# Kernel tuning notes

Measured on AMD Instinct MI355X. Metric: run time of the kernel, lower is better.

## Reference

```python
import jax, jax.numpy as jnp
import numpy as np

D_MODEL = 1024
N_HEADS = 16
HEAD_DIM = D_MODEL // N_HEADS
MASKED_BIAS = -10000.0


def setup_inputs() -> dict:
    key = jax.random.key(0)
    k1, k2, k3 = jax.random.split(key, 3)
    B, S = 2, 2048
    hidden_states = jax.random.normal(k1, (B, S, D_MODEL), dtype=jnp.float32)
    c_attn_w = jax.random.normal(k2, (D_MODEL, 3 * D_MODEL), dtype=jnp.float32) * 0.02
    c_attn_b = jnp.zeros((3 * D_MODEL,), dtype=jnp.float32)
    c_proj_w = jax.random.normal(k3, (D_MODEL, D_MODEL), dtype=jnp.float32) * 0.02
    c_proj_b = jnp.zeros((D_MODEL,), dtype=jnp.float32)
    return {
        "hidden_states": hidden_states,
        "c_attn_w": c_attn_w,
        "c_attn_b": c_attn_b,
        "c_proj_w": c_proj_w,
        "c_proj_b": c_proj_b,
    }


def reference(hidden_states, c_attn_w, c_attn_b, c_proj_w, c_proj_b):
    B, S, D = hidden_states.shape
    qkv = hidden_states @ c_attn_w + c_attn_b  # [B, S, 3D]
    q, k, v = jnp.split(qkv, 3, axis=-1)
    # split heads -> [B, H, S, Dh]
    def split_heads(t):
        return t.reshape(B, S, N_HEADS, HEAD_DIM).transpose(0, 2, 1, 3)
    q, k, v = split_heads(q), split_heads(k), split_heads(v)
    attn_weights = jnp.einsum("bhqd,bhkd->bhqk", q, k)
    attn_weights = attn_weights / jnp.asarray(float(HEAD_DIM) ** 0.5, attn_weights.dtype)
    causal_mask = jnp.tril(jnp.ones((S, S), dtype=bool))[None, None]
    attn_weights = jnp.where(causal_mask, attn_weights, jnp.asarray(MASKED_BIAS, attn_weights.dtype))
    attn_weights = jax.nn.softmax(attn_weights, axis=-1)
    attn_output = jnp.einsum("bhqk,bhkd->bhqd", attn_weights, v)
    attn_output = attn_output.transpose(0, 2, 1, 3).reshape(B, S, D)
    attn_output = attn_output @ c_proj_w + c_proj_b
    return attn_output, attn_weights
```

## Files before the change

### kernel.cpp

```cpp
#include <hip/hip_runtime.h>
#include <hip/hip_bf16.h>

#define BB 2
#define SS 2048
#define DD 1024
#define HH 16
#define DH 64
#define N3 3072

typedef __hip_bfloat16 bf16;
typedef __attribute__((ext_vector_type(8))) short short8;
typedef __attribute__((ext_vector_type(4))) short short4v;
typedef __attribute__((ext_vector_type(4))) float f32x4;

__device__ __forceinline__ float b2f(bf16 x) { return __bfloat162float(x); }

__device__ __forceinline__ short f2bs(float x) {
    bf16 t = __float2bfloat16(x);
    return *reinterpret_cast<short*>(&t);
}

__global__ __launch_bounds__(256) void split_f32(const float* __restrict__ x,
                                                 bf16* __restrict__ hi,
                                                 bf16* __restrict__ lo, int n4) {
    int idx = blockIdx.x * 256 + threadIdx.x;
    const int stride = gridDim.x * 256;
    for (int i = idx; i < n4; i += stride) {
        f32x4 v = ((const f32x4*)x)[i];
        short4v h, l;
        #pragma unroll
        for (int j = 0; j < 4; ++j) {
            bf16 hh = __float2bfloat16(v[j]);
            h[j] = *reinterpret_cast<short*>(&hh);
            float lof = v[j] - b2f(hh);
            l[j] = f2bs(lof);
        }
        ((short4v*)hi)[i] = h;
        ((short4v*)lo)[i] = l;
    }
}

__global__ __launch_bounds__(256) void transpose_split(const float* __restrict__ W,
                                                       bf16* __restrict__ Th,
                                                       bf16* __restrict__ Tl,
                                                       int K, int N) {
    __shared__ float t[64][65];
    const int k0 = blockIdx.y * 64, n0 = blockIdx.x * 64;
    const int c = threadIdx.x & 63, r4 = threadIdx.x >> 6;
    #pragma unroll
    for (int i = 0; i < 16; ++i) {
        int r = i * 4 + r4;
        t[r][c] = W[(size_t)(k0 + r) * N + n0 + c];
    }
    __syncthreads();
    #pragma unroll
    for (int i = 0; i < 16; ++i) {
        int r = i * 4 + r4;
        float x = t[c][r];
        bf16 h = __float2bfloat16(x);
        float lof = x - b2f(h);
        Th[(size_t)(n0 + r) * K + k0 + c] = h;
        Tl[(size_t)(n0 + r) * K + k0 + c] = __float2bfloat16(lof);
    }
}

__global__ __launch_bounds__(256) void qkv_mfma(const bf16* __restrict__ Ah,
                                                const bf16* __restrict__ Al,
                                                const bf16* __restrict__ Bh,
                                                const bf16* __restrict__ Bl,
                                                const float* __restrict__ bias,
                                                bf16* __restrict__ Qh,
                                                bf16* __restrict__ Kh,
                                                bf16* __restrict__ Vt) {
    const int nwg = (N3 / 128) * ((BB * SS) / 128);
    const int orig = blockIdx.x;
    const int swz = (orig & 7) * (nwg >> 3) + (orig >> 3);
    const int bx = swz % (N3 / 128), by = swz / (N3 / 128);
    const int m0 = by * 128, n0 = bx * 128;

    const int tid = threadIdx.x;
    const int lane = tid & 63;
    const int w = tid >> 6;
    const int wr = w >> 1, wc = w & 1;
    const int g = lane >> 4, lr = lane & 15;

    f32x4 acc[4][4];
    #pragma unroll
    for (int i = 0; i < 4; ++i)
        #pragma unroll
        for (int j = 0; j < 4; ++j) acc[i][j] = (f32x4){0.f, 0.f, 0.f, 0.f};

    const size_t arow = (size_t)(m0 + wr * 64 + lr) * DD;
    const size_t brow = (size_t)(n0 + wc * 64 + lr) * DD;

    for (int k0 = 0; k0 < DD; k0 += 32) {
        const int ko = k0 + g * 8;
        short8 ah[4], al[4], bhf[4], blf[4];
        #pragma unroll
        for (int i = 0; i < 4; ++i) {
            ah[i] = *(const short8*)(Ah + arow + (size_t)i * 16 * DD + ko);
            al[i] = *(const short8*)(Al + arow + (size_t)i * 16 * DD + ko);
        }
        #pragma unroll
        for (int j = 0; j < 4; ++j) {
            bhf[j] = *(const short8*)(Bh + brow + (size_t)j * 16 * DD + ko);
            blf[j] = *(const short8*)(Bl + brow + (size_t)j * 16 * DD + ko);
        }
        #pragma unroll
        for (int i = 0; i < 4; ++i)
            #pragma unroll
            for (int j = 0; j < 4; ++j) {
                acc[i][j] = __builtin_amdgcn_mfma_f32_16x16x32_bf16(ah[i], bhf[j], acc[i][j], 0, 0, 0);
                acc[i][j] = __builtin_amdgcn_mfma_f32_16x16x32_bf16(ah[i], blf[j], acc[i][j], 0, 0, 0);
                acc[i][j] = __builtin_amdgcn_mfma_f32_16x16x32_bf16(al[i], bhf[j], acc[i][j], 0, 0, 0);
            }
    }

    #pragma unroll
    for (int j = 0; j < 4; ++j) {
        const int n = n0 + wc * 64 + j * 16 + lr;
        const float bn = bias[n];
        const int which = n >> 10;
        const int d = n & 1023;
        const int h = d >> 6, dh = d & 63;
        #pragma unroll
        for (int i = 0; i < 4; ++i) {
            #pragma unroll
            for (int r = 0; r < 4; ++r) {
                const int m = m0 + wr * 64 + i * 16 + g * 4 + r;
                const int b_ = m >> 11, s = m & 2047;
                const int bh = b_ * HH + h;
                const float v = acc[i][j][r] + bn;
                if (which == 0) {
                    Qh[((size_t)bh * SS + s) * DH + dh] = __float2bfloat16(v * 0.125f);
                } else if (which == 1) {
                    Kh[((size_t)bh * SS + s) * DH + dh] = __float2bfloat16(v);
                } else {
                    Vt[((size_t)bh * DH + dh) * SS + s] = __float2bfloat16(v);
                }
            }
        }
    }
}

__global__ __launch_bounds__(64) void attn_mfma(const bf16* __restrict__ Qh,
                                                const bf16* __restrict__ Kh,
                                                const bf16* __restrict__ Vt,
                                                float* __restrict__ Wout,
                                                bf16* __restrict__ Hh) {
    const int lane = threadIdx.x;
    const int g = lane >> 4;
    const int lr = lane & 15;
    const int idx = blockIdx.x;
    const int bh = idx & 31;
    const int t = 127 - (idx >> 5);
    const int qw = t * 16;
    const int nkt = (t >> 2) + 1;

    __shared__ short pb16[1024];
    char* pb = (char*)pb16;

    short8 qf0, qf1;
    {
        const bf16* qp = Qh + ((size_t)bh * SS + qw + lr) * DH + g * 8;
        qf0 = *(const short8*)(qp);
        qf1 = *(const short8*)(qp + 32);
    }

    float lsum[4] = {0.f, 0.f, 0.f, 0.f};
    for (int kt = 0; kt < nkt; ++kt) {
        const int kbase = kt * 64;
        const bf16* kt_ptr = Kh + ((size_t)bh * SS + kbase) * DH;
        const bool diag = (kt == nkt - 1);
        f32x4 acc[4];
        #pragma unroll
        for (int ct = 0; ct < 4; ++ct) {
            const bf16* kp = kt_ptr + (size_t)(ct * 16 + lr) * DH + g * 8;
            short8 b0 = *(const short8*)(kp);
            short8 b1 = *(const short8*)(kp + 32);
            f32x4 a = {0.f, 0.f, 0.f, 0.f};
            a = __builtin_amdgcn_mfma_f32_16x16x32_bf16(qf0, b0, a, 0, 0, 0);
            a = __builtin_amdgcn_mfma_f32_16x16x32_bf16(qf1, b1, a, 0, 0, 0);
            acc[ct] = a;
        }
        #pragma unroll
        for (int r = 0; r < 4; ++r) {
            const int qrow = qw + g * 4 + r;
            float e = 0.f;
            #pragma unroll
            for (int ct = 0; ct < 4; ++ct) {
                float ev = __expf(acc[ct][r]);
                if (diag && (kbase + ct * 16 + lr) > qrow) ev = 0.f;
                e += ev;
            }
            lsum[r] += e;
        }
    }
    float inv[4];
    #pragma unroll
    for (int r = 0; r < 4; ++r) {
        float s = lsum[r];
        s += __shfl_xor(s, 1, 64);
        s += __shfl_xor(s, 2, 64);
        s += __shfl_xor(s, 4, 64);
        s += __shfl_xor(s, 8, 64);
        inv[r] = 1.f / s;
    }

    f32x4 oacc[4];
    #pragma unroll
    for (int ct = 0; ct < 4; ++ct) oacc[ct] = (f32x4){0.f, 0.f, 0.f, 0.f};

    const size_t wbase = ((size_t)bh * SS + qw) * SS;

    for (int kt = 0; kt < nkt; ++kt) {
        const int kbase = kt * 64;
        const bf16* kt_ptr = Kh + ((size_t)bh * SS + kbase) * DH;
        const bool diag = (kt == nkt - 1);
        #pragma unroll
        for (int ct = 0; ct < 4; ++ct) {
            const bf16* kp = kt_ptr + (size_t)(ct * 16 + lr) * DH + g * 8;
            short8 b0 = *(const short8*)(kp);
            short8 b1 = *(const short8*)(kp + 32);
            f32x4 a = {0.f, 0.f, 0.f, 0.f};
            a = __builtin_amdgcn_mfma_f32_16x16x32_bf16(qf0, b0, a, 0, 0, 0);
            a = __builtin_amdgcn_mfma_f32_16x16x32_bf16(qf1, b1, a, 0, 0, 0);
            #pragma unroll
            for (int r = 0; r < 4; ++r) {
                const int qrow = qw + g * 4 + r;
                const int kcol = kbase + ct * 16 + lr;
                float p = __expf(a[r]) * inv[r];
                if (diag && kcol > qrow) p = 0.f;
                Wout[wbase + (size_t)(g * 4 + r) * SS + kcol] = p;
                const int row = g * 4 + r;
                const int byte = row * 128 +
                                 (((ct * 16 + lr) * 2) ^ ((row & 7) << 4));
                *(short*)(pb + byte) = f2bs(p);
            }
        }
        __syncthreads();
        short8 pf0 = *(short8*)(pb + lr * 128 + ((g * 16) ^ ((lr & 7) << 4)));
        short8 pf1 = *(short8*)(pb + lr * 128 + ((64 + g * 16) ^ ((lr & 7) << 4)));
        const bf16* vbase = Vt + (size_t)bh * DH * SS + kbase;
        #pragma unroll
        for (int ct = 0; ct < 4; ++ct) {
            const bf16* vp = vbase + (size_t)(ct * 16 + lr) * SS + g * 8;
            short8 v0 = *(const short8*)(vp);
            short8 v1 = *(const short8*)(vp + 32);
            oacc[ct] = __builtin_amdgcn_mfma_f32_16x16x32_bf16(pf0, v0, oacc[ct], 0, 0, 0);
            oacc[ct] = __builtin_amdgcn_mfma_f32_16x16x32_bf16(pf1, v1, oacc[ct], 0, 0, 0);
        }
        __syncthreads();
    }

    #pragma unroll
    for (int ct = 0; ct < 4; ++ct) {
        #pragma unroll
        for (int r = 0; r < 4; ++r) {
            const int qrow = qw + g * 4 + r;
            const int dh = ct * 16 + lr;
            Hh[((size_t)bh * SS + qrow) * DH + dh] = __float2bfloat16(oacc[ct][r]);
        }
    }

    const int kend = nkt * 64;
    const f32x4 z = {0.f, 0.f, 0.f, 0.f};
    #pragma unroll
    for (int s = 0; s < 4; ++s) {
        const int row = (lane >> 4) + 4 * s;
        float* wr = Wout + wbase + (size_t)row * SS;
        for (int c = kend + (lane & 15) * 4; c < SS; c += 64)
            *(f32x4*)(wr + c) = z;
    }
}

__global__ __launch_bounds__(256) void proj_mfma(const bf16* __restrict__ Hh,
                                                 const bf16* __restrict__ Bh,
                                                 const bf16* __restrict__ Bl,
                                                 const float* __restrict__ bias,
                                                 float* __restrict__ out) {
    const int nwg = (DD / 128) * ((BB * SS) / 128);
    const int orig = blockIdx.x;
    const int swz = (orig & 7) * (nwg >> 3) + (orig >> 3);
    const int bx = swz % (DD / 128), by = swz / (DD / 128);
    const int m0 = by * 128, n0 = bx * 128;

    const int tid = threadIdx.x;
    const int lane = tid & 63;
    const int w = tid >> 6;
    const int wr = w >> 1, wc = w & 1;
    const int g = lane >> 4, lr = lane & 15;

    f32x4 acc[4][4];
    #pragma unroll
    for (int i = 0; i < 4; ++i)
        #pragma unroll
        for (int j = 0; j < 4; ++j) acc[i][j] = (f32x4){0.f, 0.f, 0.f, 0.f};

    const size_t brow = (size_t)(n0 + wc * 64 + lr) * DD;

    for (int k0 = 0; k0 < DD; k0 += 32) {
        const int ko = k0 + g * 8;
        const int h = ko >> 6, dho = ko & 63;
        short8 af[4], bhf[4], blf[4];
        #pragma unroll
        for (int i = 0; i < 4; ++i) {
            const int m = m0 + wr * 64 + i * 16 + lr;
            const bf16* ap = Hh + (((size_t)(m >> 11) * HH + h) * SS + (m & 2047)) * DH + dho;
            af[i] = *(const short8*)ap;
        }
        #pragma unroll
        for (int j = 0; j < 4; ++j) {
            bhf[j] = *(const short8*)(Bh + brow + (size_t)j * 16 * DD + ko);
            blf[j] = *(const short8*)(Bl + brow + (size_t)j * 16 * DD + ko);
        }
        #pragma unroll
        for (int i = 0; i < 4; ++i)
            #pragma unroll
            for (int j = 0; j < 4; ++j) {
                acc[i][j] = __builtin_amdgcn_mfma_f32_16x16x32_bf16(af[i], bhf[j], acc[i][j], 0, 0, 0);
                acc[i][j] = __builtin_amdgcn_mfma_f32_16x16x32_bf16(af[i], blf[j], acc[i][j], 0, 0, 0);
            }
    }

    #pragma unroll
    for (int j = 0; j < 4; ++j) {
        const int n = n0 + wc * 64 + j * 16 + lr;
        const float bn = bias[n];
        #pragma unroll
        for (int i = 0; i < 4; ++i) {
            #pragma unroll
            for (int r = 0; r < 4; ++r) {
                const int m = m0 + wr * 64 + i * 16 + g * 4 + r;
                out[(size_t)m * DD + n] = acc[i][j][r] + bn;
            }
        }
    }
}

extern "C" void kernel_launch(void* const* d_in, const int* in_sizes, int n_in,
                              void* d_out, int out_size, void* d_ws, size_t ws_size,
                              hipStream_t stream) {
    const float* hidden   = (const float*)d_in[0];
    const float* c_attn_w = (const float*)d_in[1];
    const float* c_attn_b = (const float*)d_in[2];
    const float* c_proj_w = (const float*)d_in[3];
    const float* c_proj_b = (const float*)d_in[4];

    float* out_attn = (float*)d_out;
    float* out_w    = (float*)d_out + (size_t)BB * SS * DD;

    const size_t NE = (size_t)BB * HH * SS * DH;
    bf16* Qh   = (bf16*)d_ws;
    bf16* Kh   = Qh + NE;
    bf16* Vt   = Kh + NE;
    bf16* Hh   = Vt + NE;
    bf16* Ahid = Hh + NE;
    bf16* Alid = Ahid + (size_t)BB * SS * DD;
    bf16* Wth  = Alid + (size_t)BB * SS * DD;
    bf16* Wtl  = Wth + (size_t)N3 * DD;
    bf16* Wpth = Wtl + (size_t)N3 * DD;
    bf16* Wptl = Wpth + (size_t)DD * DD;

    split_f32<<<dim3(1024), 256, 0, stream>>>(hidden, Ahid, Alid,
                                              (int)((size_t)BB * SS * DD / 4));
    transpose_split<<<dim3(N3 / 64, DD / 64), 256, 0, stream>>>(c_attn_w, Wth, Wtl, DD, N3);
    transpose_split<<<dim3(DD / 64, DD / 64), 256, 0, stream>>>(c_proj_w, Wpth, Wptl, DD, DD);

    qkv_mfma<<<dim3((N3 / 128) * ((BB * SS) / 128)), 256, 0, stream>>>(
        Ahid, Alid, Wth, Wtl, c_attn_b, Qh, Kh, Vt);
    attn_mfma<<<dim3(4096), 64, 0, stream>>>(
        Qh, Kh, Vt, out_w, Hh);
    proj_mfma<<<dim3((DD / 128) * ((BB * SS) / 128)), 256, 0, stream>>>(
        Hh, Wpth, Wptl, c_proj_b, out_attn);
}
```

Baseline: 1.050 ms.

## Stage GEMM operand tiles through LDS via global_load_lds in QKV and projection kernels

```diff
diff --git a/kernel.cpp b/kernel.cpp
--- a/kernel.cpp
+++ b/kernel.cpp
@@ -18,6 +18,13 @@
 __device__ __forceinline__ short f2bs(float x) {
     bf16 t = __float2bfloat16(x);
     return *reinterpret_cast<short*>(&t);
+}
+
+__device__ __forceinline__ void gld16(const bf16* gsrc, char* ldst) {
+    __builtin_amdgcn_global_load_lds(
+        (const __attribute__((address_space(1))) void*)gsrc,
+        (__attribute__((address_space(3))) void*)ldst,
+        16, 0, 0);
 }
 
 __global__ __launch_bounds__(256) void split_f32(const float* __restrict__ x,
@@ -72,6 +79,8 @@
                                                 bf16* __restrict__ Qh,
                                                 bf16* __restrict__ Kh,
                                                 bf16* __restrict__ Vt) {
+    __shared__ alignas(16) char smem[4 * 8192];
+
     const int nwg = (N3 / 128) * ((BB * SS) / 128);
     const int orig = blockIdx.x;
     const int swz = (orig & 7) * (nwg >> 3) + (orig >> 3);
@@ -83,6 +92,12 @@
     const int w = tid >> 6;
     const int wr = w >> 1, wc = w & 1;
     const int g = lane >> 4, lr = lane & 15;
+    const int sxor = lr & 3;
+
+    const bf16* const ssrc = (w == 0) ? Ah : (w == 1) ? Al : (w == 2) ? Bh : Bl;
+    const int rbase = (w < 2) ? m0 : n0;
+    char* const tbase = smem + w * 8192;
+    const int scol = (lane & 3);
 
     f32x4 acc[4][4];
     #pragma unroll
@@ -90,30 +105,40 @@
         #pragma unroll
         for (int j = 0; j < 4; ++j) acc[i][j] = (f32x4){0.f, 0.f, 0.f, 0.f};
 
-    const size_t arow = (size_t)(m0 + wr * 64 + lr) * DD;
-    const size_t brow = (size_t)(n0 + wc * 64 + lr) * DD;
-
     for (int k0 = 0; k0 < DD; k0 += 32) {
-        const int ko = k0 + g * 8;
-        short8 ah[4], al[4], bhf[4], blf[4];
+        #pragma unroll
+        for (int c = 0; c < 8; ++c) {
+            const int slot = c >> 1, rh = c & 1;
+            const int row = rh * 64 + lane;
+            gld16(ssrc + (size_t)(rbase + row) * DD + k0 + ((slot ^ scol) << 3),
+                  tbase + slot * 2048 + rh * 1024);
+        }
+        __syncthreads();
+
+        short8 ahf[4], alf[4], bhf[4], blf[4];
         #pragma unroll
         for (int i = 0; i < 4; ++i) {
-            ah[i] = *(const short8*)(Ah + arow + (size_t)i * 16 * DD + ko);
-            al[i] = *(const short8*)(Al + arow + (size_t)i * 16 * DD + ko);
+            const int ra = wr * 64 + i * 16 + lr;
+            const int off = ((g ^ sxor) << 11) + ra * 16;
+            ahf[i] = *(const short8*)(smem + off);
+            alf[i] = *(const short8*)(smem + 8192 + off);
         }
         #pragma unroll
         for (int j = 0; j < 4; ++j) {
-            bhf[j] = *(const short8*)(Bh + brow + (size_t)j * 16 * DD + ko);
-            blf[j] = *(const short8*)(Bl + brow + (size_t)j * 16 * DD + ko);
+            const int rb = wc * 64 + j * 16 + lr;
+            const int off = ((g ^ sxor) << 11) + rb * 16;
+            bhf[j] = *(const short8*)(smem + 16384 + off);
+            blf[j] = *(const short8*)(smem + 24576 + off);
         }
         #pragma unroll
         for (int i = 0; i < 4; ++i)
             #pragma unroll
             for (int j = 0; j < 4; ++j) {
-                acc[i][j] = __builtin_amdgcn_mfma_f32_16x16x32_bf16(ah[i], bhf[j], acc[i][j], 0, 0, 0);
-                acc[i][j] = __builtin_amdgcn_mfma_f32_16x16x32_bf16(ah[i], blf[j], acc[i][j], 0, 0, 0);
-                acc[i][j] = __builtin_amdgcn_mfma_f32_16x16x32_bf16(al[i], bhf[j], acc[i][j], 0, 0, 0);
-            }
+                acc[i][j] = __builtin_amdgcn_mfma_f32_16x16x32_bf16(ahf[i], bhf[j], acc[i][j], 0, 0, 0);
+                acc[i][j] = __builtin_amdgcn_mfma_f32_16x16x32_bf16(ahf[i], blf[j], acc[i][j], 0, 0, 0);
+                acc[i][j] = __builtin_amdgcn_mfma_f32_16x16x32_bf16(alf[i], bhf[j], acc[i][j], 0, 0, 0);
+            }
+        __syncthreads();
     }
 
     #pragma unroll
@@ -268,9 +293,9 @@
     #pragma unroll
     for (int s = 0; s < 4; ++s) {
         const int row = (lane >> 4) + 4 * s;
-        float* wr = Wout + wbase + (size_t)row * SS;
+        float* wr2 = Wout + wbase + (size_t)row * SS;
         for (int c = kend + (lane & 15) * 4; c < SS; c += 64)
-            *(f32x4*)(wr + c) = z;
+            *(f32x4*)(wr2 + c) = z;
     }
 }
 
@@ -279,6 +304,8 @@
                                                  const bf16* __restrict__ Bl,
                                                  const float* __restrict__ bias,
                                                  float* __restrict__ out) {
+    __shared__ alignas(16) char smem[3 * 8192];
+
     const int nwg = (DD / 128) * ((BB * SS) / 128);
     const int orig = blockIdx.x;
     const int swz = (orig & 7) * (nwg >> 3) + (orig >> 3);
@@ -290,6 +317,8 @@
     const int w = tid >> 6;
     const int wr = w >> 1, wc = w & 1;
     const int g = lane >> 4, lr = lane & 15;
+    const int sxor = lr & 3;
+    const int scol = lane & 3;
 
     f32x4 acc[4][4];
     #pragma unroll
@@ -297,22 +326,39 @@
         #pragma unroll
         for (int j = 0; j < 4; ++j) acc[i][j] = (f32x4){0.f, 0.f, 0.f, 0.f};
 
-    const size_t brow = (size_t)(n0 + wc * 64 + lr) * DD;
-
     for (int k0 = 0; k0 < DD; k0 += 32) {
-        const int ko = k0 + g * 8;
-        const int h = ko >> 6, dho = ko & 63;
+        #pragma unroll
+        for (int c = 0; c < 6; ++c) {
+            const int ch = w * 6 + c;
+            const int tile = ch >> 3;
+            const int slot = (ch & 7) >> 1, rh = ch & 1;
+            const int row = rh * 64 + lane;
+            const bf16* src;
+            if (tile == 0) {
+                const int m = m0 + row;
+                src = Hh + (((size_t)(m >> 11) * HH + (k0 >> 6)) * SS + (m & 2047)) * DH
+                        + (k0 & 63) + ((slot ^ scol) << 3);
+            } else {
+                const bf16* base = (tile == 1) ? Bh : Bl;
+                src = base + (size_t)(n0 + row) * DD + k0 + ((slot ^ scol) << 3);
+            }
+            gld16(src, smem + tile * 8192 + slot * 2048 + rh * 1024);
+        }
+        __syncthreads();
+
         short8 af[4], bhf[4], blf[4];
         #pragma unroll
         for (int i = 0; i < 4; ++i) {
-            const int m = m0 + wr * 64 + i * 16 + lr;
-            const bf16* ap = Hh + (((size_t)(m >> 11) * HH + h) * SS + (m & 2047)) * DH + dho;
-            af[i] = *(const short8*)ap;
+            const int ra = wr * 64 + i * 16 + lr;
+            const int off = ((g ^ sxor) << 11) + ra * 16;
+            af[i] = *(const short8*)(smem + off);
         }
         #pragma unroll
         for (int j = 0; j < 4; ++j) {
-            bhf[j] = *(const short8*)(Bh + brow + (size_t)j * 16 * DD + ko);
-            blf[j] = *(const short8*)(Bl + brow + (size_t)j * 16 * DD + ko);
+            const int rb = wc * 64 + j * 16 + lr;
+            const int off = ((g ^ sxor) << 11) + rb * 16;
+            bhf[j] = *(const short8*)(smem + 8192 + off);
+            blf[j] = *(const short8*)(smem + 16384 + off);
         }
         #pragma unroll
         for (int i = 0; i < 4; ++i)
@@ -321,6 +367,7 @@
                 acc[i][j] = __builtin_amdgcn_mfma_f32_16x16x32_bf16(af[i], bhf[j], acc[i][j], 0, 0, 0);
                 acc[i][j] = __builtin_amdgcn_mfma_f32_16x16x32_bf16(af[i], blf[j], acc[i][j], 0, 0, 0);
             }
+        __syncthreads();
     }
 
     #pragma unroll
```

Result: faster. 1.027 ms (-2.2%).
